# Kernel tuning notes

Hardware: AMD Instinct MI355X
Metric: run time of the kernel (lower is better)

## Reference

```python
import jax, jax.numpy as jnp
import numpy as np

D = 1024          # model dim
W = 4             # window size
H = 16
HD = D // H       # head dim
LN_EPS = 1e-5


def setup_inputs() -> dict:
    key = jax.random.key(0)
    ks = jax.random.split(key, 8)
    B, N = 4, 8192
    s = 1.0 / np.sqrt(D)
    return {
        "x": jax.random.normal(ks[0], (B, N, D), dtype=jnp.float32),
        # nn.MultiheadAttention packed in-projection: [3D, D] weight, [3D] bias
        "in_proj_w": jax.random.uniform(ks[1], (3 * D, D), minval=-s, maxval=s, dtype=jnp.float32),
        "in_proj_b": jax.random.uniform(ks[2], (3 * D,), minval=-s, maxval=s, dtype=jnp.float32),
        "out_proj_w": jax.random.uniform(ks[3], (D, D), minval=-s, maxval=s, dtype=jnp.float32),
        "out_proj_b": jnp.zeros((D,), dtype=jnp.float32),
        "ln_gamma": jnp.ones((D,), dtype=jnp.float32),
        "ln_beta": jnp.zeros((D,), dtype=jnp.float32),
        # gate is a learned scalar (init zero in torch); use nonzero so attn path is exercised
        "gate": jnp.full((1,), 0.5, dtype=jnp.float32),
    }


def _local_attn_gate(x, in_proj_w, in_proj_b, out_proj_w, out_proj_b, ln_gamma, ln_beta, gate):
    B, N, _ = x.shape
    pad = (-N) % W
    xp = jnp.pad(x, ((0, 0), (0, pad), (0, 0))) if pad else x
    Np = xp.shape[1]
    nW = Np // W

    # packed qkv projection: [B, Np, 3D]
    qkv = xp @ in_proj_w.T + in_proj_b
    q, k, v = jnp.split(qkv, 3, axis=-1)

    def to_win(t):  # [B, Np, D] -> [B, nW, W, H, HD]
        return t.reshape(B, nW, W, H, HD)

    q, k, v = to_win(q), to_win(k), to_win(v)

    scale = 1.0 / np.sqrt(HD)
    # per-window attention scores: [B, nW, H, W, W]
    scores = jnp.einsum("bnqhd,bnkhd->bnhqk", q, k) * scale
    attn = jax.nn.softmax(scores, axis=-1)
    out = jnp.einsum("bnhqk,bnkhd->bnqhd", attn, v).reshape(B, Np, D)
    out = out @ out_proj_w.T + out_proj_b
    out = out[:, :N, :]

    y = x + gate[0] * out
    mu = jnp.mean(y, axis=-1, keepdims=True)
    var = jnp.mean(jnp.square(y - mu), axis=-1, keepdims=True)
    return (y - mu) * jax.lax.rsqrt(var + LN_EPS) * ln_gamma + ln_beta


def reference(x, in_proj_w, in_proj_b, out_proj_w, out_proj_b, ln_gamma, ln_beta, gate):
    return _local_attn_gate(x, in_proj_w, in_proj_b, out_proj_w, out_proj_b, ln_gamma, ln_beta, gate)
```

## Files before the change

kernel.cpp:

```cpp
#include <hip/hip_runtime.h>
#include <stdint.h>

typedef __attribute__((ext_vector_type(8))) short short8;
typedef __attribute__((ext_vector_type(4))) float floatx4;

__device__ __forceinline__ float bf2f(uint16_t u) {
  union { uint32_t u; float f; } c; c.u = (uint32_t)u << 16; return c.f;
}
__device__ __forceinline__ uint16_t f2bf(float f) {
  union { float f; uint32_t u; } c; c.f = f;
  return (uint16_t)((c.u + 0x7fffu + ((c.u >> 16) & 1u)) >> 16);
}
__device__ __forceinline__ void gload_lds16(const void* g, void* l) {
  __builtin_amdgcn_global_load_lds(
      (const __attribute__((address_space(1))) uint32_t*)g,
      (__attribute__((address_space(3))) uint32_t*)l, 16, 0, 0);
}
__device__ __forceinline__ short8 cvt8(const float* src, size_t u) {
  const floatx4* p = (const floatx4*)src + u * 2;
  floatx4 a = p[0], b = p[1];
  short8 o;
  o[0] = (short)f2bf(a[0]); o[1] = (short)f2bf(a[1]);
  o[2] = (short)f2bf(a[2]); o[3] = (short)f2bf(a[3]);
  o[4] = (short)f2bf(b[0]); o[5] = (short)f2bf(b[1]);
  o[6] = (short)f2bf(b[2]); o[7] = (short)f2bf(b[3]);
  return o;
}

__global__ void k_cvt_all(const float* __restrict__ x, const float* __restrict__ wi,
                          const float* __restrict__ wo, const float* __restrict__ bi,
                          uint16_t* __restrict__ xb, uint16_t* __restrict__ wib,
                          uint16_t* __restrict__ wob, float* __restrict__ bip) {
  const int NX = 4194304, NWI = 393216, NWO = 131072, NB = 384;
  int i = blockIdx.x * 256 + threadIdx.x;
  if (i < NX) {
    *((short8*)xb + i) = cvt8(x, i);
  } else if (i < NX + NWI) {
    int j = i - NX;
    int row = j >> 7, cu = j & 127;
    int h = (row & 1023) >> 6, t = row >> 10, d = row & 63;
    int nrow = h * 192 + t * 64 + d;
    *((short8*)wib + (size_t)nrow * 128 + cu) = cvt8(wi, j);
  } else if (i < NX + NWI + NWO) {
    int j = i - NX - NWI;
    *((short8*)wob + j) = cvt8(wo, j);
  } else if (i < NX + NWI + NWO + NB) {
    int j = i - NX - NWI - NWO;
    int b0 = j * 8;
    int h = (b0 & 1023) >> 6, t = b0 >> 10, d = b0 & 63;
    int dst = h * 192 + t * 64 + d;
#pragma unroll
    for (int e = 0; e < 8; e++) bip[dst + e] = bi[b0 + e];
  }
}

__device__ __forceinline__ void decode_bid(int bid, int nwg, int ncols,
                                           int* mblk, int* nblk) {
  const int q = nwg >> 3;
  const int wg = (bid & 7) * q + (bid >> 3);
  *nblk = wg % ncols;
  *mblk = wg / ncols;
}

__global__ __launch_bounds__(256, 3) void k_gemm_qkv_attn(
    const uint16_t* __restrict__ A, const uint16_t* __restrict__ Wt,
    const float* __restrict__ bias, uint16_t* __restrict__ attn_o,
    int K, int nwg) {
  __shared__ __align__(16) unsigned char lds_raw[51200];
  uint16_t* lds_a  = (uint16_t*)lds_raw;
  uint16_t* lds_b  = (uint16_t*)(lds_raw + 16384);
  uint16_t* lds_ep = (uint16_t*)lds_raw;

  const int t = threadIdx.x;
  const int wave = t >> 6, lane = t & 63;
  const int wr = wave >> 1, wc = wave & 1;
  int mblk, nblk;
  decode_bid(blockIdx.x, nwg, 16, &mblk, &nblk);
  const int m0 = mblk * 128, n0 = nblk * 192;

  const char* gA = (const char*)(A + (size_t)(m0 + (t >> 2)) * K) + (t & 3) * 16;
  const char* gB = (const char*)(Wt + (size_t)(n0 + (t >> 2)) * K) + (t & 3) * 16;
  const size_t rs64 = (size_t)64 * K * 2;
  const int ksub = lane >> 4, rrow = lane & 15;
  const int nT = K / 32;

  floatx4 acc[4][6];
#pragma unroll
  for (int i = 0; i < 4; i++)
#pragma unroll
    for (int j = 0; j < 6; j++) acc[i][j] = (floatx4){0.f, 0.f, 0.f, 0.f};

  auto stage = [&](int tile) {
    char* lA = (char*)lds_a + (tile & 1) * 8192 + wave * 1024;
    char* lB = (char*)lds_b + (tile & 1) * 12288 + wave * 1024;
    const char* ga = gA + (size_t)tile * 64;
    const char* gb = gB + (size_t)tile * 64;
    gload_lds16(ga, lA);
    gload_lds16(ga + rs64, lA + 4096);
    gload_lds16(gb, lB);
    gload_lds16(gb + rs64, lB + 4096);
    gload_lds16(gb + 2 * rs64, lB + 8192);
  };

  stage(0);
  __syncthreads();
  for (int tt = 0; tt < nT; ++tt) {
    if (tt + 1 < nT) stage(tt + 1);
    const short8* pa = (const short8*)(lds_a + (tt & 1) * 4096);
    const short8* pb = (const short8*)(lds_b + (tt & 1) * 6144);
    short8 af[4], bfr[6];
#pragma unroll
    for (int i = 0; i < 4; i++)
      af[i] = pa[(wr * 64 + i * 16 + rrow) * 4 + ksub];
#pragma unroll
    for (int j = 0; j < 6; j++)
      bfr[j] = pb[(wc * 96 + j * 16 + rrow) * 4 + ksub];
#pragma unroll
    for (int i = 0; i < 4; i++)
#pragma unroll
      for (int j = 0; j < 6; j++)
        acc[i][j] = __builtin_amdgcn_mfma_f32_16x16x32_bf16(af[i], bfr[j], acc[i][j], 0, 0, 0);
    __syncthreads();
  }

  const int cq = lane >> 4, cr = lane & 15;
#pragma unroll
  for (int j = 0; j < 6; j++) {
    int col = wc * 96 + j * 16 + cr;
    float bv = bias[n0 + col];
#pragma unroll
    for (int i = 0; i < 4; i++) {
      int row = wr * 64 + i * 16 + cq * 4;
#pragma unroll
      for (int rg = 0; rg < 4; rg++)
        lds_ep[(size_t)(row + rg) * 200 + col] = f2bf(acc[i][j][rg] + bv);
    }
  }
  __syncthreads();

  const int h = nblk;
  const int g8 = lane >> 3, s8 = lane & 7;
  const int r0 = (wave * 8 + g8) * 4;
  float q[4][8], k[4][8], v[4][8];
#pragma unroll
  for (int i = 0; i < 4; i++) {
    const uint16_t* rp = lds_ep + (size_t)(r0 + i) * 200;
    short8 qv = *(const short8*)(rp + s8 * 8);
    short8 kv = *(const short8*)(rp + 64 + s8 * 8);
    short8 vv = *(const short8*)(rp + 128 + s8 * 8);
#pragma unroll
    for (int d = 0; d < 8; d++) {
      q[i][d] = bf2f((uint16_t)qv[d]);
      k[i][d] = bf2f((uint16_t)kv[d]);
      v[i][d] = bf2f((uint16_t)vv[d]);
    }
  }
  float s[4][4];
#pragma unroll
  for (int qi = 0; qi < 4; qi++)
#pragma unroll
    for (int ki = 0; ki < 4; ki++) {
      float a = 0.f;
#pragma unroll
      for (int d = 0; d < 8; d++) a = fmaf(q[qi][d], k[ki][d], a);
      s[qi][ki] = a;
    }
#pragma unroll
  for (int off = 1; off <= 4; off <<= 1)
#pragma unroll
    for (int qi = 0; qi < 4; qi++)
#pragma unroll
      for (int ki = 0; ki < 4; ki++)
        s[qi][ki] += __shfl_xor(s[qi][ki], off, 64);

#pragma unroll
  for (int qi = 0; qi < 4; qi++) {
    float a0 = s[qi][0] * 0.125f, a1 = s[qi][1] * 0.125f;
    float a2 = s[qi][2] * 0.125f, a3 = s[qi][3] * 0.125f;
    float m = fmaxf(fmaxf(a0, a1), fmaxf(a2, a3));
    float e0 = __expf(a0 - m), e1 = __expf(a1 - m);
    float e2 = __expf(a2 - m), e3 = __expf(a3 - m);
    float inv = 1.f / (e0 + e1 + e2 + e3);
    short8 ov;
#pragma unroll
    for (int d = 0; d < 8; d++) {
      float o = (e0 * v[0][d] + e1 * v[1][d] + e2 * v[2][d] + e3 * v[3][d]) * inv;
      ov[d] = (short)f2bf(o);
    }
    *(short8*)(attn_o + (size_t)(m0 + r0 + qi) * 1024 + h * 64 + s8 * 8) = ov;
  }
}

__device__ __forceinline__ void gemm_main(
    const uint16_t* __restrict__ A, const uint16_t* __restrict__ Wt, int K,
    uint16_t* lds_a, uint16_t* lds_b, int m0, int n0, floatx4 acc[4][4]) {
  const int t = threadIdx.x;
  const int wave = t >> 6, lane = t & 63;
  const int wr = wave >> 1, wc = wave & 1;
  const int r = t >> 2;
  const int cb = (t & 3) * 16;
  const char* gA = (const char*)(A + (size_t)(m0 + r) * K) + cb;
  const char* gB = (const char*)(Wt + (size_t)(n0 + r) * K) + cb;
  const size_t rowskip = (size_t)64 * K * 2;
  const int ksub = lane >> 4, rrow = lane & 15;
  const int nT = K / 32;

  {
    char* lA = (char*)lds_a + wave * 1024;
    char* lB = (char*)lds_b + wave * 1024;
    gload_lds16(gA, lA);
    gload_lds16(gA + rowskip, lA + 4096);
    gload_lds16(gB, lB);
    gload_lds16(gB + rowskip, lB + 4096);
    gA += 64; gB += 64;
  }
  __syncthreads();

  int c = 0;
  for (int tt = 0; tt < nT; ++tt) {
    if (tt + 1 < nT) {
      char* lA = (char*)lds_a + (c ^ 1) * 8192 + wave * 1024;
      char* lB = (char*)lds_b + (c ^ 1) * 8192 + wave * 1024;
      gload_lds16(gA, lA);
      gload_lds16(gA + rowskip, lA + 4096);
      gload_lds16(gB, lB);
      gload_lds16(gB + rowskip, lB + 4096);
      gA += 64; gB += 64;
    }
    const short8* pa = (const short8*)(lds_a + c * 4096);
    const short8* pb = (const short8*)(lds_b + c * 4096);
    short8 af[4], bfr[4];
#pragma unroll
    for (int i = 0; i < 4; i++)
      af[i] = pa[(wr * 64 + i * 16 + rrow) * 4 + ksub];
#pragma unroll
    for (int j = 0; j < 4; j++)
      bfr[j] = pb[(wc * 64 + j * 16 + rrow) * 4 + ksub];
#pragma unroll
    for (int i = 0; i < 4; i++)
#pragma unroll
      for (int j = 0; j < 4; j++)
        acc[i][j] = __builtin_amdgcn_mfma_f32_16x16x32_bf16(af[i], bfr[j], acc[i][j], 0, 0, 0);
    __syncthreads();
    c ^= 1;
  }
}

__global__ __launch_bounds__(256, 2) void k_gemm_out(
    const uint16_t* __restrict__ A, const uint16_t* __restrict__ Wt,
    const float* __restrict__ bias, const float* __restrict__ xres,
    const float* __restrict__ gate, uint16_t* __restrict__ Y,
    int K, int N, int nwg, int ncols) {
  __shared__ __align__(16) uint16_t lds_a[2 * 128 * 32];
  __shared__ __align__(16) uint16_t lds_b[2 * 128 * 32];
  floatx4 acc[4][4];
#pragma unroll
  for (int i = 0; i < 4; i++)
#pragma unroll
    for (int j = 0; j < 4; j++) acc[i][j] = (floatx4){0.f, 0.f, 0.f, 0.f};
  int mblk, nblk;
  decode_bid(blockIdx.x, nwg, ncols, &mblk, &nblk);
  const int m0 = mblk * 128, n0 = nblk * 128;
  gemm_main(A, Wt, K, lds_a, lds_b, m0, n0, acc);
  const float g = gate[0];
  const int wave = threadIdx.x >> 6, lane = threadIdx.x & 63;
  const int wr = wave >> 1, wc = wave & 1;
  const int cq = lane >> 4, cr = lane & 15;
#pragma unroll
  for (int j = 0; j < 4; j++) {
    int col = n0 + wc * 64 + j * 16 + cr;
    float bv = bias[col];
#pragma unroll
    for (int i = 0; i < 4; i++) {
      int row = m0 + wr * 64 + i * 16 + cq * 4;
#pragma unroll
      for (int rg = 0; rg < 4; rg++) {
        float o = acc[i][j][rg] + bv;
        float xv = xres[(size_t)(row + rg) * N + col];
        Y[(size_t)(row + rg) * N + col] = f2bf(xv + g * o);
      }
    }
  }
}

__global__ __launch_bounds__(256) void k_ln(
    const uint16_t* __restrict__ y, const float* __restrict__ gamma,
    const float* __restrict__ beta, float* __restrict__ out) {
  const int wave = threadIdx.x >> 6, lane = threadIdx.x & 63;
  const size_t row = (size_t)blockIdx.x * 4 + wave;
  const uint16_t* py = y + row * 1024 + lane * 16;
  short8 v0 = *(const short8*)py;
  short8 v1 = *(const short8*)(py + 8);
  float f[16];
#pragma unroll
  for (int j = 0; j < 8; j++) {
    f[j] = bf2f((uint16_t)v0[j]);
    f[8 + j] = bf2f((uint16_t)v1[j]);
  }
  float sum = 0.f, sq = 0.f;
#pragma unroll
  for (int j = 0; j < 16; j++) { sum += f[j]; sq += f[j] * f[j]; }
#pragma unroll
  for (int off = 32; off; off >>= 1) {
    sum += __shfl_xor(sum, off, 64);
    sq  += __shfl_xor(sq,  off, 64);
  }
  const float mu = sum * (1.f / 1024.f);
  const float var = sq * (1.f / 1024.f) - mu * mu;
  const float inv = rsqrtf(var + 1e-5f);
  const int c0 = lane * 16;
  float* po = out + row * 1024 + lane * 16;
#pragma unroll
  for (int c = 0; c < 4; c++) {
    floatx4 o;
#pragma unroll
    for (int e = 0; e < 4; e++) {
      int j = c * 4 + e;
      o[e] = (f[j] - mu) * inv * gamma[c0 + j] + beta[c0 + j];
    }
    *(floatx4*)(po + c * 4) = o;
  }
}

extern "C" void kernel_launch(void* const* d_in, const int* in_sizes, int n_in,
                              void* d_out, int out_size, void* d_ws, size_t ws_size,
                              hipStream_t stream) {
  const float* x     = (const float*)d_in[0];
  const float* w_in  = (const float*)d_in[1];
  const float* b_in  = (const float*)d_in[2];
  const float* w_out = (const float*)d_in[3];
  const float* b_out = (const float*)d_in[4];
  const float* gamma = (const float*)d_in[5];
  const float* beta  = (const float*)d_in[6];
  const float* gate  = (const float*)d_in[7];
  float* out = (float*)d_out;

  const int M = 32768;
  char* ws = (char*)d_ws;
  uint16_t* w_in_bf  = (uint16_t*)ws;
  uint16_t* w_out_bf = (uint16_t*)(ws + 6291456);
  float*    b_in_p   = (float*)(ws + 8388608);
  uint16_t* x_bf     = (uint16_t*)(ws + 8404992);
  uint16_t* attn_bf  = (uint16_t*)(ws + 8404992 + 67108864);
  uint16_t* y_bf     = (uint16_t*)(ws + 8404992 + 67108864 + 67108864);

  k_cvt_all<<<18434, 256, 0, stream>>>(x, w_in, w_out, b_in,
                                       x_bf, w_in_bf, w_out_bf, b_in_p);

  const int nwg1 = (M / 128) * 16;
  const int nwg2 = (M / 128) * (1024 / 128);
  k_gemm_qkv_attn<<<nwg1, 256, 0, stream>>>(
      x_bf, w_in_bf, b_in_p, attn_bf, 1024, nwg1);
  k_gemm_out<<<nwg2, 256, 0, stream>>>(
      attn_bf, w_out_bf, b_out, x, gate, y_bf, 1024, 1024, nwg2, 1024 / 128);
  k_ln<<<M / 4, 256, 0, stream>>>(y_bf, gamma, beta, out);
}
```

Before: 469.4 us.

## Enlarge QKV-attention tile to 256 rows with 8 waves; read residual as bf16

The fused QKV GEMM plus window-attention kernel now uses 512 threads and a 256x192 output tile, so each staged weight tile is reused across twice as many rows. The attention epilogue runs in two halves through the shared LDS buffer to fit. Separately, the output-projection kernel reads the residual from the existing bf16 copy of x instead of fp32, halving that read traffic. This costs precision on the residual add and adds extra barriers plus idle waves during the epilogue.

```diff
diff --git a/kernel.cpp b/kernel.cpp
--- a/kernel.cpp
+++ b/kernel.cpp
@@ -62,13 +62,13 @@
   *mblk = wg / ncols;
 }
 
-__global__ __launch_bounds__(256, 3) void k_gemm_qkv_attn(
+__global__ __launch_bounds__(512, 2) void k_gemm_qkv_attn(
     const uint16_t* __restrict__ A, const uint16_t* __restrict__ Wt,
     const float* __restrict__ bias, uint16_t* __restrict__ attn_o,
     int K, int nwg) {
-  __shared__ __align__(16) unsigned char lds_raw[51200];
+  __shared__ __align__(16) unsigned char lds_raw[57344];
   uint16_t* lds_a  = (uint16_t*)lds_raw;
-  uint16_t* lds_b  = (uint16_t*)(lds_raw + 16384);
+  uint16_t* lds_b  = (uint16_t*)(lds_raw + 32768);
   uint16_t* lds_ep = (uint16_t*)lds_raw;
 
   const int t = threadIdx.x;
@@ -76,11 +76,16 @@
   const int wr = wave >> 1, wc = wave & 1;
   int mblk, nblk;
   decode_bid(blockIdx.x, nwg, 16, &mblk, &nblk);
-  const int m0 = mblk * 128, n0 = nblk * 192;
-
-  const char* gA = (const char*)(A + (size_t)(m0 + (t >> 2)) * K) + (t & 3) * 16;
-  const char* gB = (const char*)(Wt + (size_t)(n0 + (t >> 2)) * K) + (t & 3) * 16;
-  const size_t rs64 = (size_t)64 * K * 2;
+  const int m0 = mblk * 256, n0 = nblk * 192;
+
+  const int sA0 = 2 * wave, sA1 = 2 * wave + 1;
+  const int sB0 = (wave < 4) ? 2 * wave : 8 + (wave - 4);
+  const int sB1 = 2 * wave + 1;
+  const int srow = lane >> 2, scol = (lane & 3) * 16;
+  const char* pA0 = (const char*)(A + (size_t)(m0 + sA0 * 16 + srow) * K) + scol;
+  const char* pA1 = (const char*)(A + (size_t)(m0 + sA1 * 16 + srow) * K) + scol;
+  const char* pB0 = (const char*)(Wt + (size_t)(n0 + sB0 * 16 + srow) * K) + scol;
+  const char* pB1 = (const char*)(Wt + (size_t)(n0 + sB1 * 16 + srow) * K) + scol;
   const int ksub = lane >> 4, rrow = lane & 15;
   const int nT = K / 32;
 
@@ -91,22 +96,20 @@
     for (int j = 0; j < 6; j++) acc[i][j] = (floatx4){0.f, 0.f, 0.f, 0.f};
 
   auto stage = [&](int tile) {
-    char* lA = (char*)lds_a + (tile & 1) * 8192 + wave * 1024;
-    char* lB = (char*)lds_b + (tile & 1) * 12288 + wave * 1024;
-    const char* ga = gA + (size_t)tile * 64;
-    const char* gb = gB + (size_t)tile * 64;
-    gload_lds16(ga, lA);
-    gload_lds16(ga + rs64, lA + 4096);
-    gload_lds16(gb, lB);
-    gload_lds16(gb + rs64, lB + 4096);
-    gload_lds16(gb + 2 * rs64, lB + 8192);
+    char* bufA = (char*)lds_a + (tile & 1) * 16384;
+    char* bufB = (char*)lds_b + (tile & 1) * 12288;
+    const size_t ko = (size_t)tile * 64;
+    gload_lds16(pA0 + ko, bufA + sA0 * 1024);
+    gload_lds16(pA1 + ko, bufA + sA1 * 1024);
+    gload_lds16(pB0 + ko, bufB + sB0 * 1024);
+    if (wave < 4) gload_lds16(pB1 + ko, bufB + sB1 * 1024);
   };
 
   stage(0);
   __syncthreads();
   for (int tt = 0; tt < nT; ++tt) {
     if (tt + 1 < nT) stage(tt + 1);
-    const short8* pa = (const short8*)(lds_a + (tt & 1) * 4096);
+    const short8* pa = (const short8*)(lds_a + (tt & 1) * 8192);
     const short8* pb = (const short8*)(lds_b + (tt & 1) * 6144);
     short8 af[4], bfr[6];
 #pragma unroll
@@ -124,70 +127,80 @@
   }
 
   const int cq = lane >> 4, cr = lane & 15;
-#pragma unroll
-  for (int j = 0; j < 6; j++) {
-    int col = wc * 96 + j * 16 + cr;
-    float bv = bias[n0 + col];
-#pragma unroll
-    for (int i = 0; i < 4; i++) {
-      int row = wr * 64 + i * 16 + cq * 4;
-#pragma unroll
-      for (int rg = 0; rg < 4; rg++)
-        lds_ep[(size_t)(row + rg) * 200 + col] = f2bf(acc[i][j][rg] + bv);
-    }
-  }
-  __syncthreads();
-
   const int h = nblk;
   const int g8 = lane >> 3, s8 = lane & 7;
-  const int r0 = (wave * 8 + g8) * 4;
-  float q[4][8], k[4][8], v[4][8];
-#pragma unroll
-  for (int i = 0; i < 4; i++) {
-    const uint16_t* rp = lds_ep + (size_t)(r0 + i) * 200;
-    short8 qv = *(const short8*)(rp + s8 * 8);
-    short8 kv = *(const short8*)(rp + 64 + s8 * 8);
-    short8 vv = *(const short8*)(rp + 128 + s8 * 8);
-#pragma unroll
-    for (int d = 0; d < 8; d++) {
-      q[i][d] = bf2f((uint16_t)qv[d]);
-      k[i][d] = bf2f((uint16_t)kv[d]);
-      v[i][d] = bf2f((uint16_t)vv[d]);
-    }
-  }
-  float s[4][4];
-#pragma unroll
-  for (int qi = 0; qi < 4; qi++)
-#pragma unroll
-    for (int ki = 0; ki < 4; ki++) {
-      float a = 0.f;
-#pragma unroll
-      for (int d = 0; d < 8; d++) a = fmaf(q[qi][d], k[ki][d], a);
-      s[qi][ki] = a;
-    }
-#pragma unroll
-  for (int off = 1; off <= 4; off <<= 1)
-#pragma unroll
-    for (int qi = 0; qi < 4; qi++)
-#pragma unroll
-      for (int ki = 0; ki < 4; ki++)
-        s[qi][ki] += __shfl_xor(s[qi][ki], off, 64);
-
-#pragma unroll
-  for (int qi = 0; qi < 4; qi++) {
-    float a0 = s[qi][0] * 0.125f, a1 = s[qi][1] * 0.125f;
-    float a2 = s[qi][2] * 0.125f, a3 = s[qi][3] * 0.125f;
-    float m = fmaxf(fmaxf(a0, a1), fmaxf(a2, a3));
-    float e0 = __expf(a0 - m), e1 = __expf(a1 - m);
-    float e2 = __expf(a2 - m), e3 = __expf(a3 - m);
-    float inv = 1.f / (e0 + e1 + e2 + e3);
-    short8 ov;
-#pragma unroll
-    for (int d = 0; d < 8; d++) {
-      float o = (e0 * v[0][d] + e1 * v[1][d] + e2 * v[2][d] + e3 * v[3][d]) * inv;
-      ov[d] = (short)f2bf(o);
-    }
-    *(short8*)(attn_o + (size_t)(m0 + r0 + qi) * 1024 + h * 64 + s8 * 8) = ov;
+#pragma unroll 1
+  for (int half = 0; half < 2; ++half) {
+    if ((wr >> 1) == half) {
+      const int wrl = wr & 1;
+#pragma unroll
+      for (int j = 0; j < 6; j++) {
+        int col = wc * 96 + j * 16 + cr;
+        float bv = bias[n0 + col];
+#pragma unroll
+        for (int i = 0; i < 4; i++) {
+          int row = wrl * 64 + i * 16 + cq * 4;
+#pragma unroll
+          for (int rg = 0; rg < 4; rg++)
+            lds_ep[(size_t)(row + rg) * 200 + col] = f2bf(acc[i][j][rg] + bv);
+        }
+      }
+    }
+    __syncthreads();
+    {
+      const int w32 = (wave & 3) * 8 + g8;
+      const int r0 = w32 * 4;
+      float q[4][8], k[4][8], v[4][8];
+#pragma unroll
+      for (int i = 0; i < 4; i++) {
+        const uint16_t* rp = lds_ep + (size_t)(r0 + i) * 200;
+        short8 qv = *(const short8*)(rp + s8 * 8);
+        short8 kv = *(const short8*)(rp + 64 + s8 * 8);
+        short8 vv = *(const short8*)(rp + 128 + s8 * 8);
+#pragma unroll
+        for (int d = 0; d < 8; d++) {
+          q[i][d] = bf2f((uint16_t)qv[d]);
+          k[i][d] = bf2f((uint16_t)kv[d]);
+          v[i][d] = bf2f((uint16_t)vv[d]);
+        }
+      }
+      float s[4][4];
+#pragma unroll
+      for (int qi = 0; qi < 4; qi++)
+#pragma unroll
+        for (int ki = 0; ki < 4; ki++) {
+          float a = 0.f;
+#pragma unroll
+          for (int d = 0; d < 8; d++) a = fmaf(q[qi][d], k[ki][d], a);
+          s[qi][ki] = a;
+        }
+#pragma unroll
+      for (int off = 1; off <= 4; off <<= 1)
+#pragma unroll
+        for (int qi = 0; qi < 4; qi++)
+#pragma unroll
+          for (int ki = 0; ki < 4; ki++)
+            s[qi][ki] += __shfl_xor(s[qi][ki], off, 64);
+      if (wave < 4) {
+#pragma unroll
+        for (int qi = 0; qi < 4; qi++) {
+          float a0 = s[qi][0] * 0.125f, a1 = s[qi][1] * 0.125f;
+          float a2 = s[qi][2] * 0.125f, a3 = s[qi][3] * 0.125f;
+          float m = fmaxf(fmaxf(a0, a1), fmaxf(a2, a3));
+          float e0 = __expf(a0 - m), e1 = __expf(a1 - m);
+          float e2 = __expf(a2 - m), e3 = __expf(a3 - m);
+          float inv = 1.f / (e0 + e1 + e2 + e3);
+          short8 ov;
+#pragma unroll
+          for (int d = 0; d < 8; d++) {
+            float o = (e0 * v[0][d] + e1 * v[1][d] + e2 * v[2][d] + e3 * v[3][d]) * inv;
+            ov[d] = (short)f2bf(o);
+          }
+          *(short8*)(attn_o + (size_t)(m0 + half * 128 + r0 + qi) * 1024 + h * 64 + s8 * 8) = ov;
+        }
+      }
+    }
+    if (half == 0) __syncthreads();
   }
 }
 
@@ -248,7 +261,7 @@
 
 __global__ __launch_bounds__(256, 2) void k_gemm_out(
     const uint16_t* __restrict__ A, const uint16_t* __restrict__ Wt,
-    const float* __restrict__ bias, const float* __restrict__ xres,
+    const float* __restrict__ bias, const uint16_t* __restrict__ xres_bf,
     const float* __restrict__ gate, uint16_t* __restrict__ Y,
     int K, int N, int nwg, int ncols) {
   __shared__ __align__(16) uint16_t lds_a[2 * 128 * 32];
@@ -276,7 +289,7 @@
 #pragma unroll
       for (int rg = 0; rg < 4; rg++) {
         float o = acc[i][j][rg] + bv;
-        float xv = xres[(size_t)(row + rg) * N + col];
+        float xv = bf2f(xres_bf[(size_t)(row + rg) * N + col]);
         Y[(size_t)(row + rg) * N + col] = f2bf(xv + g * o);
       }
     }
@@ -347,11 +360,11 @@
   k_cvt_all<<<18434, 256, 0, stream>>>(x, w_in, w_out, b_in,
                                        x_bf, w_in_bf, w_out_bf, b_in_p);
 
-  const int nwg1 = (M / 128) * 16;
+  const int nwg1 = (M / 256) * 16;
   const int nwg2 = (M / 128) * (1024 / 128);
-  k_gemm_qkv_attn<<<nwg1, 256, 0, stream>>>(
+  k_gemm_qkv_attn<<<nwg1, 512, 0, stream>>>(
       x_bf, w_in_bf, b_in_p, attn_bf, 1024, nwg1);
   k_gemm_out<<<nwg2, 256, 0, stream>>>(
-      attn_bf, w_out_bf, b_out, x, gate, y_bf, 1024, 1024, nwg2, 1024 / 128);
+      attn_bf, w_out_bf, b_out, x_bf, gate, y_bf, 1024, 1024, nwg2, 1024 / 128);
   k_ln<<<M / 4, 256, 0, stream>>>(y_bf, gamma, beta, out);
 }
```

Result: slower. 480.9 us (+2.4%).

## Split QKV-attention GEMM across 8 waves and read bf16 residual

Applied to the files above, without the earlier changes.

The fused QKV+attention kernel now launches 512 threads (8 waves). Each wave owns a 64x48 output sub-tile instead of 64x96, and the global-to-LDS staging is redistributed across the waves. Only the first four waves write the attention output, so the other four do redundant epilogue math. Separately, the out-projection epilogue reads the residual from the bf16 copy of x instead of fp32, which halves that read traffic at some cost in precision.

```diff
diff --git a/kernel.cpp b/kernel.cpp
--- a/kernel.cpp
+++ b/kernel.cpp
@@ -62,7 +62,7 @@
   *mblk = wg / ncols;
 }
 
-__global__ __launch_bounds__(256, 3) void k_gemm_qkv_attn(
+__global__ __launch_bounds__(512, 2) void k_gemm_qkv_attn(
     const uint16_t* __restrict__ A, const uint16_t* __restrict__ Wt,
     const float* __restrict__ bias, uint16_t* __restrict__ attn_o,
     int K, int nwg) {
@@ -73,33 +73,31 @@
 
   const int t = threadIdx.x;
   const int wave = t >> 6, lane = t & 63;
-  const int wr = wave >> 1, wc = wave & 1;
+  const int wr = wave & 1, wc = wave >> 1;
   int mblk, nblk;
   decode_bid(blockIdx.x, nwg, 16, &mblk, &nblk);
   const int m0 = mblk * 128, n0 = nblk * 192;
 
-  const char* gA = (const char*)(A + (size_t)(m0 + (t >> 2)) * K) + (t & 3) * 16;
-  const char* gB = (const char*)(Wt + (size_t)(n0 + (t >> 2)) * K) + (t & 3) * 16;
-  const size_t rs64 = (size_t)64 * K * 2;
+  const int srow = lane >> 2, scol = (lane & 3) * 16;
+  const char* pA0 = (const char*)(A + (size_t)(m0 + wave * 16 + srow) * K) + scol;
+  const char* pB0 = (const char*)(Wt + (size_t)(n0 + wave * 16 + srow) * K) + scol;
+  const char* pB1 = (const char*)(Wt + (size_t)(n0 + (8 + (wave - 4)) * 16 + srow) * K) + scol;
   const int ksub = lane >> 4, rrow = lane & 15;
   const int nT = K / 32;
 
-  floatx4 acc[4][6];
+  floatx4 acc[4][3];
 #pragma unroll
   for (int i = 0; i < 4; i++)
 #pragma unroll
-    for (int j = 0; j < 6; j++) acc[i][j] = (floatx4){0.f, 0.f, 0.f, 0.f};
+    for (int j = 0; j < 3; j++) acc[i][j] = (floatx4){0.f, 0.f, 0.f, 0.f};
 
   auto stage = [&](int tile) {
-    char* lA = (char*)lds_a + (tile & 1) * 8192 + wave * 1024;
-    char* lB = (char*)lds_b + (tile & 1) * 12288 + wave * 1024;
-    const char* ga = gA + (size_t)tile * 64;
-    const char* gb = gB + (size_t)tile * 64;
-    gload_lds16(ga, lA);
-    gload_lds16(ga + rs64, lA + 4096);
-    gload_lds16(gb, lB);
-    gload_lds16(gb + rs64, lB + 4096);
-    gload_lds16(gb + 2 * rs64, lB + 8192);
+    char* bufA = (char*)lds_a + (tile & 1) * 8192;
+    char* bufB = (char*)lds_b + (tile & 1) * 12288;
+    const size_t ko = (size_t)tile * 64;
+    gload_lds16(pA0 + ko, bufA + wave * 1024);
+    gload_lds16(pB0 + ko, bufB + wave * 1024);
+    if (wave >= 4) gload_lds16(pB1 + ko, bufB + (8 + (wave - 4)) * 1024);
   };
 
   stage(0);
@@ -108,25 +106,25 @@
     if (tt + 1 < nT) stage(tt + 1);
     const short8* pa = (const short8*)(lds_a + (tt & 1) * 4096);
     const short8* pb = (const short8*)(lds_b + (tt & 1) * 6144);
-    short8 af[4], bfr[6];
+    short8 af[4], bfr[3];
 #pragma unroll
     for (int i = 0; i < 4; i++)
       af[i] = pa[(wr * 64 + i * 16 + rrow) * 4 + ksub];
 #pragma unroll
-    for (int j = 0; j < 6; j++)
-      bfr[j] = pb[(wc * 96 + j * 16 + rrow) * 4 + ksub];
+    for (int j = 0; j < 3; j++)
+      bfr[j] = pb[(wc * 48 + j * 16 + rrow) * 4 + ksub];
 #pragma unroll
     for (int i = 0; i < 4; i++)
 #pragma unroll
-      for (int j = 0; j < 6; j++)
+      for (int j = 0; j < 3; j++)
         acc[i][j] = __builtin_amdgcn_mfma_f32_16x16x32_bf16(af[i], bfr[j], acc[i][j], 0, 0, 0);
     __syncthreads();
   }
 
   const int cq = lane >> 4, cr = lane & 15;
 #pragma unroll
-  for (int j = 0; j < 6; j++) {
-    int col = wc * 96 + j * 16 + cr;
+  for (int j = 0; j < 3; j++) {
+    int col = wc * 48 + j * 16 + cr;
     float bv = bias[n0 + col];
 #pragma unroll
     for (int i = 0; i < 4; i++) {
@@ -140,7 +138,8 @@
 
   const int h = nblk;
   const int g8 = lane >> 3, s8 = lane & 7;
-  const int r0 = (wave * 8 + g8) * 4;
+  const int w32 = (wave & 3) * 8 + g8;
+  const int r0 = w32 * 4;
   float q[4][8], k[4][8], v[4][8];
 #pragma unroll
   for (int i = 0; i < 4; i++) {
@@ -172,22 +171,23 @@
 #pragma unroll
       for (int ki = 0; ki < 4; ki++)
         s[qi][ki] += __shfl_xor(s[qi][ki], off, 64);
-
-#pragma unroll
-  for (int qi = 0; qi < 4; qi++) {
-    float a0 = s[qi][0] * 0.125f, a1 = s[qi][1] * 0.125f;
-    float a2 = s[qi][2] * 0.125f, a3 = s[qi][3] * 0.125f;
-    float m = fmaxf(fmaxf(a0, a1), fmaxf(a2, a3));
-    float e0 = __expf(a0 - m), e1 = __expf(a1 - m);
-    float e2 = __expf(a2 - m), e3 = __expf(a3 - m);
-    float inv = 1.f / (e0 + e1 + e2 + e3);
-    short8 ov;
-#pragma unroll
-    for (int d = 0; d < 8; d++) {
-      float o = (e0 * v[0][d] + e1 * v[1][d] + e2 * v[2][d] + e3 * v[3][d]) * inv;
-      ov[d] = (short)f2bf(o);
-    }
-    *(short8*)(attn_o + (size_t)(m0 + r0 + qi) * 1024 + h * 64 + s8 * 8) = ov;
+  if (wave < 4) {
+#pragma unroll
+    for (int qi = 0; qi < 4; qi++) {
+      float a0 = s[qi][0] * 0.125f, a1 = s[qi][1] * 0.125f;
+      float a2 = s[qi][2] * 0.125f, a3 = s[qi][3] * 0.125f;
+      float m = fmaxf(fmaxf(a0, a1), fmaxf(a2, a3));
+      float e0 = __expf(a0 - m), e1 = __expf(a1 - m);
+      float e2 = __expf(a2 - m), e3 = __expf(a3 - m);
+      float inv = 1.f / (e0 + e1 + e2 + e3);
+      short8 ov;
+#pragma unroll
+      for (int d = 0; d < 8; d++) {
+        float o = (e0 * v[0][d] + e1 * v[1][d] + e2 * v[2][d] + e3 * v[3][d]) * inv;
+        ov[d] = (short)f2bf(o);
+      }
+      *(short8*)(attn_o + (size_t)(m0 + r0 + qi) * 1024 + h * 64 + s8 * 8) = ov;
+    }
   }
 }
 
@@ -248,7 +248,7 @@
 
 __global__ __launch_bounds__(256, 2) void k_gemm_out(
     const uint16_t* __restrict__ A, const uint16_t* __restrict__ Wt,
-    const float* __restrict__ bias, const float* __restrict__ xres,
+    const float* __restrict__ bias, const uint16_t* __restrict__ xres_bf,
     const float* __restrict__ gate, uint16_t* __restrict__ Y,
     int K, int N, int nwg, int ncols) {
   __shared__ __align__(16) uint16_t lds_a[2 * 128 * 32];
@@ -276,7 +276,7 @@
 #pragma unroll
       for (int rg = 0; rg < 4; rg++) {
         float o = acc[i][j][rg] + bv;
-        float xv = xres[(size_t)(row + rg) * N + col];
+        float xv = bf2f(xres_bf[(size_t)(row + rg) * N + col]);
         Y[(size_t)(row + rg) * N + col] = f2bf(xv + g * o);
       }
     }
@@ -349,9 +349,9 @@
 
   const int nwg1 = (M / 128) * 16;
   const int nwg2 = (M / 128) * (1024 / 128);
-  k_gemm_qkv_attn<<<nwg1, 256, 0, stream>>>(
+  k_gemm_qkv_attn<<<nwg1, 512, 0, stream>>>(
       x_bf, w_in_bf, b_in_p, attn_bf, 1024, nwg1);
   k_gemm_out<<<nwg2, 256, 0, stream>>>(
-      attn_bf, w_out_bf, b_out, x, gate, y_bf, 1024, 1024, nwg2, 1024 / 128);
+      attn_bf, w_out_bf, b_out, x_bf, gate, y_bf, 1024, 1024, nwg2, 1024 / 128);
   k_ln<<<M / 4, 256, 0, stream>>>(y_bf, gamma, beta, out);
 }
```

Result: faster. 457.7 us (-2.5%).
